# Performance work log

Hardware: AMD Instinct MI355X
Metric: run time of the kernel (lower is better)

Reference implementation:

```python
import jax, jax.numpy as jnp
import numpy as np

N = 50000        # nodes
E = 800000       # edges (avg degree 16)
IN = 128         # in_feats
HF = 128         # h_feats
HID = (IN + HF) // 2  # 128, per math.floor((h_feats+in_feats)/2)


def setup_inputs() -> dict:
    key = jax.random.key(0)
    ks = jax.random.split(key, 13)

    def glorot(k, fan_in, fan_out):
        s = (2.0 / (fan_in + fan_out)) ** 0.5
        return jax.random.normal(k, (fan_in, fan_out), jnp.float32) * s

    dims = [(IN, HID), (HID, HID), (HID, HID), (HID, HID), (HID, HF)]
    inp = {
        "in_feat": jax.random.normal(ks[0], (N, IN), jnp.float32),
        "src": jax.random.randint(ks[1], (E,), 0, N),
        "dst": jax.random.randint(ks[2], (E,), 0, N),
    }
    for i, (a, b) in enumerate(dims):
        inp[f"W{i+1}"] = glorot(ks[3 + i], a, b)
        inp[f"b{i+1}"] = jnp.zeros((b,), jnp.float32)
    return inp


def reference(in_feat, src, dst, W1, W2, W3, W4, W5, b1, b2, b3, b4, b5):
    # DGL GraphConv, norm='both': y = D_in^{-1/2} * A^T * (D_out^{-1/2} * x) @ W + b
    ones = jnp.ones((src.shape[0],), in_feat.dtype)
    deg_out = jnp.clip(jax.ops.segment_sum(ones, src, num_segments=N), 1.0)
    deg_in = jnp.clip(jax.ops.segment_sum(ones, dst, num_segments=N), 1.0)
    ns = (deg_out ** -0.5)[:, None]  # source-side norm [N,1]
    nd = (deg_in ** -0.5)[:, None]   # dest-side norm   [N,1]

    def conv(x, W, b):
        m = jax.ops.segment_sum((x * ns)[src], dst, num_segments=N)  # [N,D]
        return (m * nd) @ W + b

    h = in_feat
    for W, b in ((W1, b1), (W2, b2), (W3, b3), (W4, b4), (W5, b5)):
        h = jax.nn.relu(conv(h, W, b))

    # vectorized version of the per-element Python double loop threshold
    h_clone = jnp.where(h >= 0.5, jnp.float32(1.0), jnp.float32(0.0))
    return h, h_clone
```

## Files before the change

kernel.cpp:

```cpp
#include <hip/hip_runtime.h>

#define FEAT 128
#define RANGE 12800
#define NSLICE 64

typedef _Float16 half8 __attribute__((ext_vector_type(8)));
typedef _Float16 half4v __attribute__((ext_vector_type(4)));
typedef float f32x4 __attribute__((ext_vector_type(4)));

__global__ __launch_bounds__(1024) void hist_kernel(const int* __restrict__ src,
                                                    const int* __restrict__ dst,
                                                    unsigned* __restrict__ partialD,
                                                    unsigned* __restrict__ partialS,
                                                    int E, int NP) {
    __shared__ unsigned hpk[RANGE / 2];
    int per = (NP / RANGE) * NSLICE;
    int b = blockIdx.x;
    int halfsel = b / per;
    int q = b % per;
    int r = q / NSLICE;
    int s = q % NSLICE;
    const int* arr = halfsel ? src : dst;
    unsigned* out = halfsel ? partialS : partialD;
    int v0 = r * RANGE;
    int tid = threadIdx.x;
    for (int i = tid; i < RANGE / 2; i += 1024) hpk[i] = 0;
    __syncthreads();
    int e0 = (int)((long long)E * s / NSLICE);
    int e1 = (int)((long long)E * (s + 1) / NSLICE);
    for (int e = e0 + tid; e < e1; e += 1024) {
        unsigned d = (unsigned)(arr[e] - v0);
        if (d < RANGE) atomicAdd(&hpk[d >> 1], (d & 1) ? 65536u : 1u);
    }
    __syncthreads();
    size_t wbase = ((size_t)s * NP + v0) >> 1;
    for (int i = tid; i < RANGE / 2; i += 1024) out[wbase + i] = hpk[i];
}

__global__ __launch_bounds__(256) void scanp1_kernel(const unsigned short* __restrict__ pD,
                                                     const unsigned short* __restrict__ pS,
                                                     int* __restrict__ blockSums,
                                                     float* __restrict__ ns,
                                                     float* __restrict__ nd,
                                                     int NP, int n) {
    __shared__ int buf[256];
    int tid = threadIdx.x;
    int v = blockIdx.x * 256 + tid;
    int ssum = 0, osum = 0;
    #pragma unroll
    for (int s = 0; s < NSLICE; ++s) {
        ssum += pD[(size_t)s * NP + v];
        osum += pS[(size_t)s * NP + v];
    }
    if (v < n) {
        ns[v] = 1.0f / sqrtf((float)(osum < 1 ? 1 : osum));
        nd[v] = 1.0f / sqrtf((float)(ssum < 1 ? 1 : ssum));
    }
    buf[tid] = ssum;
    __syncthreads();
    #pragma unroll
    for (int off = 1; off < 256; off <<= 1) {
        int t = (tid >= off) ? buf[tid - off] : 0;
        __syncthreads();
        buf[tid] += t;
        __syncthreads();
    }
    if (tid == 255) blockSums[blockIdx.x] = buf[255];
}

__global__ __launch_bounds__(256) void scanp2_kernel(const int* __restrict__ blockSums,
                                                     int* __restrict__ blockOffs, int nb) {
    __shared__ int buf[256];
    int tid = threadIdx.x;
    int v = (tid < nb) ? blockSums[tid] : 0;
    buf[tid] = v;
    __syncthreads();
    #pragma unroll
    for (int off = 1; off < 256; off <<= 1) {
        int t = (tid >= off) ? buf[tid - off] : 0;
        __syncthreads();
        buf[tid] += t;
        __syncthreads();
    }
    if (tid < nb) blockOffs[tid] = buf[tid] - v;
}

__global__ __launch_bounds__(256) void scanp3_kernel(const unsigned short* __restrict__ pD,
                                                     const int* __restrict__ blockOffs,
                                                     int* __restrict__ cursorV,
                                                     int* __restrict__ offsc,
                                                     int NP, int n) {
    __shared__ int buf[256];
    int tid = threadIdx.x;
    int v = blockIdx.x * 256 + tid;
    int ssum = 0;
    #pragma unroll
    for (int s = 0; s < NSLICE; ++s) ssum += pD[(size_t)s * NP + v];
    buf[tid] = ssum;
    __syncthreads();
    #pragma unroll
    for (int off = 1; off < 256; off <<= 1) {
        int t = (tid >= off) ? buf[tid - off] : 0;
        __syncthreads();
        buf[tid] += t;
        __syncthreads();
    }
    int o = blockOffs[blockIdx.x] + buf[tid] - ssum;
    if (v <= n) offsc[v] = o;
    int* cv = cursorV + (size_t)v * NSLICE;
    #pragma unroll
    for (int s = 0; s < NSLICE; ++s) {
        int val = pD[(size_t)s * NP + v];
        cv[s] = o;
        o += val;
    }
}

__global__ __launch_bounds__(1024) void fill_kernel(const int* __restrict__ src,
                                                    const int* __restrict__ dst,
                                                    const int* __restrict__ cursorV,
                                                    int* __restrict__ esrc, int E, int NP) {
    __shared__ int cur[RANGE];
    int b = blockIdx.x;
    int r = b / NSLICE;
    int inner = b % NSLICE;
    int s = ((inner & 7) << 3) | (inner >> 3);
    int v0 = r * RANGE;
    int tid = threadIdx.x;
    for (int i = tid; i < RANGE; i += 1024)
        cur[i] = cursorV[(size_t)(v0 + i) * NSLICE + s];
    __syncthreads();
    int e0 = (int)((long long)E * s / NSLICE);
    int e1 = (int)((long long)E * (s + 1) / NSLICE);
    for (int e = e0 + tid; e < e1; e += 1024) {
        unsigned dd = (unsigned)(dst[e] - v0);
        if (dd < RANGE) {
            int p = atomicAdd(&cur[dd], 1);
            esrc[p] = src[e];
        }
    }
}

__global__ void prescale_kernel(const float* __restrict__ x, const float* __restrict__ ns,
                                _Float16* __restrict__ xh, int n) {
    int i = blockIdx.x * blockDim.x + threadIdx.x;
    if (i >= n * (FEAT / 8)) return;
    int v = i >> 4;
    float w = ns[v];
    float4 t0 = ((const float4*)x)[i * 2];
    float4 t1 = ((const float4*)x)[i * 2 + 1];
    half8 h;
    h[0] = (_Float16)(t0.x * w); h[1] = (_Float16)(t0.y * w);
    h[2] = (_Float16)(t0.z * w); h[3] = (_Float16)(t0.w * w);
    h[4] = (_Float16)(t1.x * w); h[5] = (_Float16)(t1.y * w);
    h[6] = (_Float16)(t1.z * w); h[7] = (_Float16)(t1.w * w);
    ((float4*)xh)[i] = __builtin_bit_cast(float4, h);
}

__global__ __launch_bounds__(256) void wprep_kernel(const float* __restrict__ Wa,
                                                    const float* __restrict__ Wb,
                                                    const float* __restrict__ Wc,
                                                    const float* __restrict__ Wd,
                                                    const float* __restrict__ We,
                                                    _Float16* __restrict__ w16t,
                                                    _Float16* __restrict__ wrt) {
    int gid = blockIdx.x * 256 + threadIdx.x;
    int l = gid >> 14;
    int idx = gid & 16383;
    int col = idx >> 7;
    int k = idx & 127;
    const float* Wp = (l == 0) ? Wa : (l == 1) ? Wb : (l == 2) ? Wc : (l == 3) ? Wd : We;
    float w = Wp[k * FEAT + col];
    _Float16 h = (_Float16)w;
    _Float16 r = (_Float16)(w - (float)h);
    w16t[gid] = h;
    wrt[gid] = r;
}

__global__ __launch_bounds__(256) void agg_kernel(const _Float16* __restrict__ x,
                                                  const int* __restrict__ offs,
                                                  const int* __restrict__ esrc,
                                                  const float* __restrict__ nd,
                                                  float* __restrict__ m, int n) {
    int gid = blockIdx.x * blockDim.x + threadIdx.x;
    int v = gid >> 6;
    if (v >= n) return;
    int lane = threadIdx.x & 63;
    int q = lane >> 4;
    int c = lane & 15;
    int s0 = offs[v], s1 = offs[v + 1];
    float a0[8] = {0,0,0,0,0,0,0,0};
    float a1[8] = {0,0,0,0,0,0,0,0};
    float a2[8] = {0,0,0,0,0,0,0,0};
    float a3[8] = {0,0,0,0,0,0,0,0};
    int j = s0 + q;
    for (; j + 12 < s1; j += 16) {
        int e0 = esrc[j], e1 = esrc[j + 4], e2 = esrc[j + 8], e3 = esrc[j + 12];
        float4 r0 = ((const float4*)(x + (size_t)e0 * FEAT))[c];
        float4 r1 = ((const float4*)(x + (size_t)e1 * FEAT))[c];
        float4 r2 = ((const float4*)(x + (size_t)e2 * FEAT))[c];
        float4 r3 = ((const float4*)(x + (size_t)e3 * FEAT))[c];
        half8 h0 = __builtin_bit_cast(half8, r0);
        half8 h1 = __builtin_bit_cast(half8, r1);
        half8 h2 = __builtin_bit_cast(half8, r2);
        half8 h3 = __builtin_bit_cast(half8, r3);
        #pragma unroll
        for (int k = 0; k < 8; ++k) {
            a0[k] += (float)h0[k];
            a1[k] += (float)h1[k];
            a2[k] += (float)h2[k];
            a3[k] += (float)h3[k];
        }
    }
    for (; j < s1; j += 4) {
        int e0 = esrc[j];
        float4 r0 = ((const float4*)(x + (size_t)e0 * FEAT))[c];
        half8 h0 = __builtin_bit_cast(half8, r0);
        #pragma unroll
        for (int k = 0; k < 8; ++k) a0[k] += (float)h0[k];
    }
    float r[8];
    #pragma unroll
    for (int k = 0; k < 8; ++k) r[k] = (a0[k] + a1[k]) + (a2[k] + a3[k]);
    #pragma unroll
    for (int k = 0; k < 8; ++k) {
        r[k] += __shfl_xor(r[k], 16);
        r[k] += __shfl_xor(r[k], 32);
    }
    if (lane < 16) {
        float sc = nd[v];
        float4 o0, o1;
        o0.x = r[0] * sc; o0.y = r[1] * sc; o0.z = r[2] * sc; o0.w = r[3] * sc;
        o1.x = r[4] * sc; o1.y = r[5] * sc; o1.z = r[6] * sc; o1.w = r[7] * sc;
        ((float4*)(m + (size_t)v * FEAT))[c * 2] = o0;
        ((float4*)(m + (size_t)v * FEAT))[c * 2 + 1] = o1;
    }
}

template<int MODE>
__global__ __launch_bounds__(256) void gemm_kernel(const float* __restrict__ M,
                                                   const _Float16* __restrict__ w16t,
                                                   const _Float16* __restrict__ wrt,
                                                   const float* __restrict__ bias,
                                                   const float* __restrict__ nsv,
                                                   _Float16* __restrict__ outh,
                                                   float* __restrict__ outf,
                                                   float* __restrict__ out2, int n) {
    __shared__ _Float16 A16s[32 * 128];
    __shared__ _Float16 Ars[32 * 128];
    __shared__ _Float16 W16s[128 * 128];
    __shared__ _Float16 Wrs[128 * 128];
    int tid = threadIdx.x;
    int r0 = blockIdx.x * 32;

    #pragma unroll
    for (int j = 0; j < 8; ++j) {
        int i = tid + j * 256;
        int col = i >> 4, ch = i & 15;
        int d = col * 16 + (ch ^ (col & 7));
        ((float4*)W16s)[d] = ((const float4*)w16t)[i];
        ((float4*)Wrs)[d]  = ((const float4*)wrt)[i];
    }
    #pragma unroll
    for (int j = 0; j < 4; ++j) {
        int i = tid + j * 256;
        int row = i >> 5, c4 = i & 31;
        int gr = r0 + row;
        float4 v = make_float4(0.f, 0.f, 0.f, 0.f);
        if (gr < n) v = ((const float4*)(M + (size_t)gr * FEAT))[c4];
        half4v h, rr;
        h[0] = (_Float16)v.x; h[1] = (_Float16)v.y; h[2] = (_Float16)v.z; h[3] = (_Float16)v.w;
        rr[0] = (_Float16)(v.x - (float)h[0]); rr[1] = (_Float16)(v.y - (float)h[1]);
        rr[2] = (_Float16)(v.z - (float)h[2]); rr[3] = (_Float16)(v.w - (float)h[3]);
        int d = row * 128 + (((c4 >> 1) ^ (row & 7)) << 3) + ((c4 & 1) << 2);
        *(half4v*)(A16s + d) = h;
        *(half4v*)(Ars + d) = rr;
    }
    __syncthreads();

    int lane = tid & 63;
    int w = tid >> 6;
    int l15 = lane & 15;
    int q = lane >> 4;
    int rbase = (w & 1) * 16 + l15;
    int cbase = (w >> 1) * 64;

    f32x4 acc[4] = {{0.f,0.f,0.f,0.f},{0.f,0.f,0.f,0.f},{0.f,0.f,0.f,0.f},{0.f,0.f,0.f,0.f}};
    #pragma unroll
    for (int ks = 0; ks < 4; ++ks) {
        int chunk = ks * 4 + q;
        int aoff = rbase * 128 + ((chunk ^ (rbase & 7)) << 3);
        half8 a16 = *(const half8*)(A16s + aoff);
        half8 ar  = *(const half8*)(Ars + aoff);
        #pragma unroll
        for (int ct = 0; ct < 4; ++ct) {
            int col = cbase + ct * 16 + l15;
            int boff = col * 128 + ((chunk ^ (col & 7)) << 3);
            half8 b16 = *(const half8*)(W16s + boff);
            half8 br  = *(const half8*)(Wrs + boff);
            acc[ct] = __builtin_amdgcn_mfma_f32_16x16x32_f16(a16, b16, acc[ct], 0, 0, 0);
            acc[ct] = __builtin_amdgcn_mfma_f32_16x16x32_f16(a16, br,  acc[ct], 0, 0, 0);
            acc[ct] = __builtin_amdgcn_mfma_f32_16x16x32_f16(ar,  b16, acc[ct], 0, 0, 0);
        }
    }

    int rloc = (w & 1) * 16 + q * 4;
    float scv[4];
    #pragma unroll
    for (int reg = 0; reg < 4; ++reg) {
        int row = r0 + rloc + reg;
        scv[reg] = (MODE == 0 && row < n) ? nsv[row] : 1.0f;
    }
    #pragma unroll
    for (int ct = 0; ct < 4; ++ct) {
        int col = cbase + ct * 16 + l15;
        float b = bias[col];
        #pragma unroll
        for (int reg = 0; reg < 4; ++reg) {
            int row = r0 + rloc + reg;
            if (row < n) {
                float h = acc[ct][reg] + b;
                h = h > 0.f ? h : 0.f;
                if (MODE == 0) {
                    outh[(size_t)row * FEAT + col] = (_Float16)(h * scv[reg]);
                } else {
                    outf[(size_t)row * FEAT + col] = h;
                    out2[(size_t)row * FEAT + col] = h >= 0.5f ? 1.f : 0.f;
                }
            }
        }
    }
}

extern "C" void kernel_launch(void* const* d_in, const int* in_sizes, int n_in,
                              void* d_out, int out_size, void* d_ws, size_t ws_size,
                              hipStream_t stream) {
    const float* in_feat = (const float*)d_in[0];
    const int*   src     = (const int*)d_in[1];
    const int*   dst     = (const int*)d_in[2];
    const float* W[5] = {(const float*)d_in[3], (const float*)d_in[5], (const float*)d_in[7],
                         (const float*)d_in[9], (const float*)d_in[11]};
    const float* B[5] = {(const float*)d_in[4], (const float*)d_in[6], (const float*)d_in[8],
                         (const float*)d_in[10], (const float*)d_in[12]};
    const int E = in_sizes[1];
    const int N = in_sizes[0] / FEAT;
    const int NRANGE = (N + RANGE - 1) / RANGE;
    const int NP = NRANGE * RANGE;
    const size_t MTOT = (size_t)NP * NSLICE;

    char* ws = (char*)d_ws;
    size_t off = 0;
    auto alloc = [&](size_t bytes) { size_t o = off; off += (bytes + 255) & ~size_t(255); return o; };
    unsigned* partialD = (unsigned*)(ws + alloc(MTOT * 2));
    size_t    pS_off   = alloc(MTOT * 2);
    unsigned* partialS = (unsigned*)(ws + pS_off);
    int*      esrc     = (int*)(ws + pS_off);
    size_t    cV_off   = alloc(MTOT * 4);
    int*      cursorV  = (int*)(ws + cV_off);
    _Float16* xh       = (_Float16*)(ws + cV_off);
    float*    ns       = (float*)(ws + alloc((size_t)N * 4));
    float*    nd       = (float*)(ws + alloc((size_t)N * 4));
    int*      offsc    = (int*)(ws + alloc((size_t)(N + 1) * 4));
    int*      blockSums = (int*)(ws + alloc(1024));
    int*      blockOffs = (int*)(ws + alloc(1024));
    _Float16* w16t     = (_Float16*)(ws + alloc(5 * 16384 * 2));
    _Float16* wrt      = (_Float16*)(ws + alloc(5 * 16384 * 2));

    float* out_h = (float*)d_out;
    float* out_c = out_h + (size_t)N * FEAT;

    const int histBlocks = 2 * NRANGE * NSLICE;
    const int scanBlocks = NP / 256;
    hist_kernel<<<histBlocks, 1024, 0, stream>>>(src, dst, partialD, partialS, E, NP);
    scanp1_kernel<<<scanBlocks, 256, 0, stream>>>((const unsigned short*)partialD,
                                                  (const unsigned short*)partialS,
                                                  blockSums, ns, nd, NP, N);
    scanp2_kernel<<<1, 256, 0, stream>>>(blockSums, blockOffs, scanBlocks);
    scanp3_kernel<<<scanBlocks, 256, 0, stream>>>((const unsigned short*)partialD,
                                                  blockOffs, cursorV, offsc, NP, N);
    fill_kernel<<<NRANGE * NSLICE, 1024, 0, stream>>>(src, dst, cursorV, esrc, E, NP);
    wprep_kernel<<<320, 256, 0, stream>>>(W[0], W[1], W[2], W[3], W[4], w16t, wrt);
    prescale_kernel<<<(N * (FEAT / 8) + 255) / 256, 256, 0, stream>>>(in_feat, ns, xh, N);

    const int agg_blocks = (int)(((size_t)N * 64 + 255) / 256);
    const int gemm_blocks = (N + 31) / 32;

    for (int l = 0; l < 5; ++l) {
        agg_kernel<<<agg_blocks, 256, 0, stream>>>(xh, offsc, esrc, nd, out_h, N);
        if (l < 4)
            gemm_kernel<0><<<gemm_blocks, 256, 0, stream>>>(out_h, w16t + (size_t)l * 16384,
                                                            wrt + (size_t)l * 16384, B[l], ns,
                                                            xh, nullptr, nullptr, N);
        else
            gemm_kernel<1><<<gemm_blocks, 256, 0, stream>>>(out_h, w16t + (size_t)l * 16384,
                                                            wrt + (size_t)l * 16384, B[l], nullptr,
                                                            nullptr, out_h, out_c, N);
    }
}
```

Measured before the change: 465.5 us.

## Fuse neighbor aggregation and dense GEMM into one per-layer kernel

Merges the aggregation kernel and the MFMA GEMM kernel into a single kernel per layer. Aggregated rows for a 64-node tile are kept in shared memory as fp32, then split into fp16 hi/lo and fed to the MFMAs, which removes the fp32 round trip of the aggregate through global memory and one launch per layer. Weights are now read straight from global memory instead of being staged in LDS. Ping-pong fp16 feature buffers are added because the layer now reads and writes features in the same kernel, at the cost of an extra N×128 workspace buffer.

```diff
diff --git a/kernel.cpp b/kernel.cpp
--- a/kernel.cpp
+++ b/kernel.cpp
@@ -5,7 +5,6 @@
 #define NSLICE 64
 
 typedef _Float16 half8 __attribute__((ext_vector_type(8)));
-typedef _Float16 half4v __attribute__((ext_vector_type(4)));
 typedef float f32x4 __attribute__((ext_vector_type(4)));
 
 __global__ __launch_bounds__(1024) void hist_kernel(const int* __restrict__ src,
@@ -177,134 +176,118 @@
     wrt[gid] = r;
 }
 
-__global__ __launch_bounds__(256) void agg_kernel(const _Float16* __restrict__ x,
-                                                  const int* __restrict__ offs,
-                                                  const int* __restrict__ esrc,
-                                                  const float* __restrict__ nd,
-                                                  float* __restrict__ m, int n) {
-    int gid = blockIdx.x * blockDim.x + threadIdx.x;
-    int v = gid >> 6;
-    if (v >= n) return;
-    int lane = threadIdx.x & 63;
+template<int MODE>
+__global__ __launch_bounds__(512, 4) void fused_kernel(const _Float16* __restrict__ x,
+                                                       const int* __restrict__ offs,
+                                                       const int* __restrict__ esrc,
+                                                       const float* __restrict__ nd,
+                                                       const float* __restrict__ nsv,
+                                                       const _Float16* __restrict__ w16t,
+                                                       const _Float16* __restrict__ wrt,
+                                                       const float* __restrict__ bias,
+                                                       _Float16* __restrict__ outh,
+                                                       float* __restrict__ outf,
+                                                       float* __restrict__ out2, int n) {
+    __shared__ float ms[64][132];
+    int tid = threadIdx.x;
+    int r0 = blockIdx.x * 64;
+
+    int hw = tid >> 5;
+    int lane = tid & 31;
     int q = lane >> 4;
     int c = lane & 15;
-    int s0 = offs[v], s1 = offs[v + 1];
-    float a0[8] = {0,0,0,0,0,0,0,0};
-    float a1[8] = {0,0,0,0,0,0,0,0};
-    float a2[8] = {0,0,0,0,0,0,0,0};
-    float a3[8] = {0,0,0,0,0,0,0,0};
-    int j = s0 + q;
-    for (; j + 12 < s1; j += 16) {
-        int e0 = esrc[j], e1 = esrc[j + 4], e2 = esrc[j + 8], e3 = esrc[j + 12];
-        float4 r0 = ((const float4*)(x + (size_t)e0 * FEAT))[c];
-        float4 r1 = ((const float4*)(x + (size_t)e1 * FEAT))[c];
-        float4 r2 = ((const float4*)(x + (size_t)e2 * FEAT))[c];
-        float4 r3 = ((const float4*)(x + (size_t)e3 * FEAT))[c];
-        half8 h0 = __builtin_bit_cast(half8, r0);
-        half8 h1 = __builtin_bit_cast(half8, r1);
-        half8 h2 = __builtin_bit_cast(half8, r2);
-        half8 h3 = __builtin_bit_cast(half8, r3);
-        #pragma unroll
-        for (int k = 0; k < 8; ++k) {
-            a0[k] += (float)h0[k];
-            a1[k] += (float)h1[k];
-            a2[k] += (float)h2[k];
-            a3[k] += (float)h3[k];
+    #pragma unroll
+    for (int t = 0; t < 4; ++t) {
+        int row = hw * 4 + t;
+        int v = r0 + row;
+        if (v < n) {
+            int s0 = offs[v], s1 = offs[v + 1];
+            float a0[8] = {0,0,0,0,0,0,0,0};
+            float a1[8] = {0,0,0,0,0,0,0,0};
+            float a2[8] = {0,0,0,0,0,0,0,0};
+            float a3[8] = {0,0,0,0,0,0,0,0};
+            int j = s0 + q;
+            for (; j + 6 < s1; j += 8) {
+                int e0 = esrc[j], e1 = esrc[j + 2], e2 = esrc[j + 4], e3 = esrc[j + 6];
+                float4 r0v = ((const float4*)(x + (size_t)e0 * FEAT))[c];
+                float4 r1v = ((const float4*)(x + (size_t)e1 * FEAT))[c];
+                float4 r2v = ((const float4*)(x + (size_t)e2 * FEAT))[c];
+                float4 r3v = ((const float4*)(x + (size_t)e3 * FEAT))[c];
+                half8 h0 = __builtin_bit_cast(half8, r0v);
+                half8 h1 = __builtin_bit_cast(half8, r1v);
+                half8 h2 = __builtin_bit_cast(half8, r2v);
+                half8 h3 = __builtin_bit_cast(half8, r3v);
+                #pragma unroll
+                for (int k = 0; k < 8; ++k) {
+                    a0[k] += (float)h0[k];
+                    a1[k] += (float)h1[k];
+                    a2[k] += (float)h2[k];
+                    a3[k] += (float)h3[k];
+                }
+            }
+            for (; j < s1; j += 2) {
+                int e0 = esrc[j];
+                float4 r0v = ((const float4*)(x + (size_t)e0 * FEAT))[c];
+                half8 h0 = __builtin_bit_cast(half8, r0v);
+                #pragma unroll
+                for (int k = 0; k < 8; ++k) a0[k] += (float)h0[k];
+            }
+            float r[8];
+            #pragma unroll
+            for (int k = 0; k < 8; ++k) r[k] = (a0[k] + a1[k]) + (a2[k] + a3[k]);
+            #pragma unroll
+            for (int k = 0; k < 8; ++k) r[k] += __shfl_xor(r[k], 16);
+            if (q == 0) {
+                float sc = nd[v];
+                float4 o0, o1;
+                o0.x = r[0] * sc; o0.y = r[1] * sc; o0.z = r[2] * sc; o0.w = r[3] * sc;
+                o1.x = r[4] * sc; o1.y = r[5] * sc; o1.z = r[6] * sc; o1.w = r[7] * sc;
+                *(float4*)&ms[row][c * 8] = o0;
+                *(float4*)&ms[row][c * 8 + 4] = o1;
+            }
+        } else if (q == 0) {
+            float4 z = make_float4(0.f, 0.f, 0.f, 0.f);
+            *(float4*)&ms[row][c * 8] = z;
+            *(float4*)&ms[row][c * 8 + 4] = z;
         }
     }
-    for (; j < s1; j += 4) {
-        int e0 = esrc[j];
-        float4 r0 = ((const float4*)(x + (size_t)e0 * FEAT))[c];
-        half8 h0 = __builtin_bit_cast(half8, r0);
-        #pragma unroll
-        for (int k = 0; k < 8; ++k) a0[k] += (float)h0[k];
-    }
-    float r[8];
-    #pragma unroll
-    for (int k = 0; k < 8; ++k) r[k] = (a0[k] + a1[k]) + (a2[k] + a3[k]);
-    #pragma unroll
-    for (int k = 0; k < 8; ++k) {
-        r[k] += __shfl_xor(r[k], 16);
-        r[k] += __shfl_xor(r[k], 32);
-    }
-    if (lane < 16) {
-        float sc = nd[v];
-        float4 o0, o1;
-        o0.x = r[0] * sc; o0.y = r[1] * sc; o0.z = r[2] * sc; o0.w = r[3] * sc;
-        o1.x = r[4] * sc; o1.y = r[5] * sc; o1.z = r[6] * sc; o1.w = r[7] * sc;
-        ((float4*)(m + (size_t)v * FEAT))[c * 2] = o0;
-        ((float4*)(m + (size_t)v * FEAT))[c * 2 + 1] = o1;
-    }
-}
-
-template<int MODE>
-__global__ __launch_bounds__(256) void gemm_kernel(const float* __restrict__ M,
-                                                   const _Float16* __restrict__ w16t,
-                                                   const _Float16* __restrict__ wrt,
-                                                   const float* __restrict__ bias,
-                                                   const float* __restrict__ nsv,
-                                                   _Float16* __restrict__ outh,
-                                                   float* __restrict__ outf,
-                                                   float* __restrict__ out2, int n) {
-    __shared__ _Float16 A16s[32 * 128];
-    __shared__ _Float16 Ars[32 * 128];
-    __shared__ _Float16 W16s[128 * 128];
-    __shared__ _Float16 Wrs[128 * 128];
-    int tid = threadIdx.x;
-    int r0 = blockIdx.x * 32;
-
-    #pragma unroll
-    for (int j = 0; j < 8; ++j) {
-        int i = tid + j * 256;
-        int col = i >> 4, ch = i & 15;
-        int d = col * 16 + (ch ^ (col & 7));
-        ((float4*)W16s)[d] = ((const float4*)w16t)[i];
-        ((float4*)Wrs)[d]  = ((const float4*)wrt)[i];
-    }
-    #pragma unroll
-    for (int j = 0; j < 4; ++j) {
-        int i = tid + j * 256;
-        int row = i >> 5, c4 = i & 31;
-        int gr = r0 + row;
-        float4 v = make_float4(0.f, 0.f, 0.f, 0.f);
-        if (gr < n) v = ((const float4*)(M + (size_t)gr * FEAT))[c4];
-        half4v h, rr;
-        h[0] = (_Float16)v.x; h[1] = (_Float16)v.y; h[2] = (_Float16)v.z; h[3] = (_Float16)v.w;
-        rr[0] = (_Float16)(v.x - (float)h[0]); rr[1] = (_Float16)(v.y - (float)h[1]);
-        rr[2] = (_Float16)(v.z - (float)h[2]); rr[3] = (_Float16)(v.w - (float)h[3]);
-        int d = row * 128 + (((c4 >> 1) ^ (row & 7)) << 3) + ((c4 & 1) << 2);
-        *(half4v*)(A16s + d) = h;
-        *(half4v*)(Ars + d) = rr;
-    }
-    __syncthreads();
-
-    int lane = tid & 63;
+    __syncthreads();
+
+    int lane64 = tid & 63;
     int w = tid >> 6;
-    int l15 = lane & 15;
-    int q = lane >> 4;
-    int rbase = (w & 1) * 16 + l15;
-    int cbase = (w >> 1) * 64;
+    int l15 = lane64 & 15;
+    int qq = lane64 >> 4;
+    int rw = w & 3, cw = w >> 2;
+    int rbase = rw * 16 + l15;
+    int cbase = cw * 64;
 
     f32x4 acc[4] = {{0.f,0.f,0.f,0.f},{0.f,0.f,0.f,0.f},{0.f,0.f,0.f,0.f},{0.f,0.f,0.f,0.f}};
     #pragma unroll
     for (int ks = 0; ks < 4; ++ks) {
-        int chunk = ks * 4 + q;
-        int aoff = rbase * 128 + ((chunk ^ (rbase & 7)) << 3);
-        half8 a16 = *(const half8*)(A16s + aoff);
-        half8 ar  = *(const half8*)(Ars + aoff);
+        int chunk = ks * 4 + qq;
+        float4 f0 = *(const float4*)&ms[rbase][chunk * 8];
+        float4 f1 = *(const float4*)&ms[rbase][chunk * 8 + 4];
+        half8 a16, ar;
+        a16[0] = (_Float16)f0.x; a16[1] = (_Float16)f0.y;
+        a16[2] = (_Float16)f0.z; a16[3] = (_Float16)f0.w;
+        a16[4] = (_Float16)f1.x; a16[5] = (_Float16)f1.y;
+        a16[6] = (_Float16)f1.z; a16[7] = (_Float16)f1.w;
+        ar[0] = (_Float16)(f0.x - (float)a16[0]); ar[1] = (_Float16)(f0.y - (float)a16[1]);
+        ar[2] = (_Float16)(f0.z - (float)a16[2]); ar[3] = (_Float16)(f0.w - (float)a16[3]);
+        ar[4] = (_Float16)(f1.x - (float)a16[4]); ar[5] = (_Float16)(f1.y - (float)a16[5]);
+        ar[6] = (_Float16)(f1.z - (float)a16[6]); ar[7] = (_Float16)(f1.w - (float)a16[7]);
         #pragma unroll
         for (int ct = 0; ct < 4; ++ct) {
             int col = cbase + ct * 16 + l15;
-            int boff = col * 128 + ((chunk ^ (col & 7)) << 3);
-            half8 b16 = *(const half8*)(W16s + boff);
-            half8 br  = *(const half8*)(Wrs + boff);
+            half8 b16 = *(const half8*)(w16t + (size_t)col * FEAT + chunk * 8);
+            half8 br  = *(const half8*)(wrt  + (size_t)col * FEAT + chunk * 8);
             acc[ct] = __builtin_amdgcn_mfma_f32_16x16x32_f16(a16, b16, acc[ct], 0, 0, 0);
             acc[ct] = __builtin_amdgcn_mfma_f32_16x16x32_f16(a16, br,  acc[ct], 0, 0, 0);
             acc[ct] = __builtin_amdgcn_mfma_f32_16x16x32_f16(ar,  b16, acc[ct], 0, 0, 0);
         }
     }
 
-    int rloc = (w & 1) * 16 + q * 4;
+    int rloc = rw * 16 + qq * 4;
     float scv[4];
     #pragma unroll
     for (int reg = 0; reg < 4; ++reg) {
@@ -357,7 +340,7 @@
     int*      esrc     = (int*)(ws + pS_off);
     size_t    cV_off   = alloc(MTOT * 4);
     int*      cursorV  = (int*)(ws + cV_off);
-    _Float16* xh       = (_Float16*)(ws + cV_off);
+    _Float16* xhA      = (_Float16*)(ws + cV_off);
     float*    ns       = (float*)(ws + alloc((size_t)N * 4));
     float*    nd       = (float*)(ws + alloc((size_t)N * 4));
     int*      offsc    = (int*)(ws + alloc((size_t)(N + 1) * 4));
@@ -365,6 +348,7 @@
     int*      blockOffs = (int*)(ws + alloc(1024));
     _Float16* w16t     = (_Float16*)(ws + alloc(5 * 16384 * 2));
     _Float16* wrt      = (_Float16*)(ws + alloc(5 * 16384 * 2));
+    _Float16* xhB      = (_Float16*)(ws + alloc((size_t)N * FEAT * 2));
 
     float* out_h = (float*)d_out;
     float* out_c = out_h + (size_t)N * FEAT;
@@ -380,20 +364,22 @@
                                                   blockOffs, cursorV, offsc, NP, N);
     fill_kernel<<<NRANGE * NSLICE, 1024, 0, stream>>>(src, dst, cursorV, esrc, E, NP);
     wprep_kernel<<<320, 256, 0, stream>>>(W[0], W[1], W[2], W[3], W[4], w16t, wrt);
-    prescale_kernel<<<(N * (FEAT / 8) + 255) / 256, 256, 0, stream>>>(in_feat, ns, xh, N);
-
-    const int agg_blocks = (int)(((size_t)N * 64 + 255) / 256);
-    const int gemm_blocks = (N + 31) / 32;
+    prescale_kernel<<<(N * (FEAT / 8) + 255) / 256, 256, 0, stream>>>(in_feat, ns, xhA, N);
+
+    const int fusedBlocks = (N + 63) / 64;
 
     for (int l = 0; l < 5; ++l) {
-        agg_kernel<<<agg_blocks, 256, 0, stream>>>(xh, offsc, esrc, nd, out_h, N);
+        const _Float16* xin = (l & 1) ? xhB : xhA;
+        _Float16*       xout = (l & 1) ? xhA : xhB;
         if (l < 4)
-            gemm_kernel<0><<<gemm_blocks, 256, 0, stream>>>(out_h, w16t + (size_t)l * 16384,
-                                                            wrt + (size_t)l * 16384, B[l], ns,
-                                                            xh, nullptr, nullptr, N);
+            fused_kernel<0><<<fusedBlocks, 512, 0, stream>>>(xin, offsc, esrc, nd, ns,
+                                                             w16t + (size_t)l * 16384,
+                                                             wrt + (size_t)l * 16384, B[l],
+                                                             xout, nullptr, nullptr, N);
         else
-            gemm_kernel<1><<<gemm_blocks, 256, 0, stream>>>(out_h, w16t + (size_t)l * 16384,
-                                                            wrt + (size_t)l * 16384, B[l], nullptr,
-                                                            nullptr, out_h, out_c, N);
-    }
-}
+            fused_kernel<1><<<fusedBlocks, 512, 0, stream>>>(xin, offsc, esrc, nd, nullptr,
+                                                             w16t + (size_t)l * 16384,
+                                                             wrt + (size_t)l * 16384, B[l],
+                                                             nullptr, out_h, out_c, N);
+    }
+}
```

New measurement: 514.0 us. +10.4%, slower.

## Merge prep kernels and read GEMM weights from global instead of LDS

Applied to the files above, without the earlier changes.

Folds the weight-prep work into the first scan kernel and merges the block-sum scan into the third scan kernel, so the preprocessing chain issues two fewer launches. The GEMM kernel now uses 512 threads on 64-row tiles and stops staging the two 128x128 fp16 weight tiles in shared memory. B fragments are loaded straight from global/L2 instead, which cuts LDS use from about 80KB to 32KB per block and allows more resident blocks. The trade-off is more scattered global loads of the weight matrices inside the MFMA loop, and every prep2 block redundantly rescans the block sums.

```diff
diff --git a/kernel.cpp b/kernel.cpp
--- a/kernel.cpp
+++ b/kernel.cpp
@@ -37,26 +37,69 @@
     for (int i = tid; i < RANGE / 2; i += 1024) out[wbase + i] = hpk[i];
 }
 
-__global__ __launch_bounds__(256) void scanp1_kernel(const unsigned short* __restrict__ pD,
-                                                     const unsigned short* __restrict__ pS,
-                                                     int* __restrict__ blockSums,
-                                                     float* __restrict__ ns,
-                                                     float* __restrict__ nd,
-                                                     int NP, int n) {
+__global__ __launch_bounds__(256) void prep1_kernel(const unsigned short* __restrict__ pD,
+                                                    const unsigned short* __restrict__ pS,
+                                                    int* __restrict__ blockSums,
+                                                    float* __restrict__ ns,
+                                                    float* __restrict__ nd,
+                                                    const float* __restrict__ Wa,
+                                                    const float* __restrict__ Wb,
+                                                    const float* __restrict__ Wc,
+                                                    const float* __restrict__ Wd,
+                                                    const float* __restrict__ We,
+                                                    _Float16* __restrict__ w16t,
+                                                    _Float16* __restrict__ wrt,
+                                                    int NP, int n, int sb) {
+    int tid = threadIdx.x;
+    int b = blockIdx.x;
+    if (b < sb) {
+        __shared__ int buf[256];
+        int v = b * 256 + tid;
+        int ssum = 0, osum = 0;
+        #pragma unroll
+        for (int s = 0; s < NSLICE; ++s) {
+            ssum += pD[(size_t)s * NP + v];
+            osum += pS[(size_t)s * NP + v];
+        }
+        if (v < n) {
+            ns[v] = 1.0f / sqrtf((float)(osum < 1 ? 1 : osum));
+            nd[v] = 1.0f / sqrtf((float)(ssum < 1 ? 1 : ssum));
+        }
+        buf[tid] = ssum;
+        __syncthreads();
+        #pragma unroll
+        for (int off = 1; off < 256; off <<= 1) {
+            int t = (tid >= off) ? buf[tid - off] : 0;
+            __syncthreads();
+            buf[tid] += t;
+            __syncthreads();
+        }
+        if (tid == 255) blockSums[b] = buf[255];
+    } else {
+        int gid = (b - sb) * 256 + tid;
+        int l = gid >> 14;
+        int idx = gid & 16383;
+        int col = idx >> 7;
+        int k = idx & 127;
+        const float* Wp = (l == 0) ? Wa : (l == 1) ? Wb : (l == 2) ? Wc : (l == 3) ? Wd : We;
+        float w = Wp[k * FEAT + col];
+        _Float16 h = (_Float16)w;
+        _Float16 r = (_Float16)(w - (float)h);
+        w16t[gid] = h;
+        wrt[gid] = r;
+    }
+}
+
+__global__ __launch_bounds__(256) void prep2_kernel(const unsigned short* __restrict__ pD,
+                                                    const int* __restrict__ blockSums,
+                                                    int* __restrict__ cursorV,
+                                                    int* __restrict__ offsc,
+                                                    int NP, int n, int nb) {
     __shared__ int buf[256];
     int tid = threadIdx.x;
-    int v = blockIdx.x * 256 + tid;
-    int ssum = 0, osum = 0;
-    #pragma unroll
-    for (int s = 0; s < NSLICE; ++s) {
-        ssum += pD[(size_t)s * NP + v];
-        osum += pS[(size_t)s * NP + v];
-    }
-    if (v < n) {
-        ns[v] = 1.0f / sqrtf((float)(osum < 1 ? 1 : osum));
-        nd[v] = 1.0f / sqrtf((float)(ssum < 1 ? 1 : ssum));
-    }
-    buf[tid] = ssum;
+    int b = blockIdx.x;
+    int bsv = (tid < nb) ? blockSums[tid] : 0;
+    buf[tid] = bsv;
     __syncthreads();
     #pragma unroll
     for (int off = 1; off < 256; off <<= 1) {
@@ -65,15 +108,13 @@
         buf[tid] += t;
         __syncthreads();
     }
-    if (tid == 255) blockSums[blockIdx.x] = buf[255];
-}
-
-__global__ __launch_bounds__(256) void scanp2_kernel(const int* __restrict__ blockSums,
-                                                     int* __restrict__ blockOffs, int nb) {
-    __shared__ int buf[256];
-    int tid = threadIdx.x;
-    int v = (tid < nb) ? blockSums[tid] : 0;
-    buf[tid] = v;
+    int myoff = (b > 0) ? buf[b - 1] : 0;
+    __syncthreads();
+    int v = b * 256 + tid;
+    int ssum = 0;
+    #pragma unroll
+    for (int s = 0; s < NSLICE; ++s) ssum += pD[(size_t)s * NP + v];
+    buf[tid] = ssum;
     __syncthreads();
     #pragma unroll
     for (int off = 1; off < 256; off <<= 1) {
@@ -82,30 +123,7 @@
         buf[tid] += t;
         __syncthreads();
     }
-    if (tid < nb) blockOffs[tid] = buf[tid] - v;
-}
-
-__global__ __launch_bounds__(256) void scanp3_kernel(const unsigned short* __restrict__ pD,
-                                                     const int* __restrict__ blockOffs,
-                                                     int* __restrict__ cursorV,
-                                                     int* __restrict__ offsc,
-                                                     int NP, int n) {
-    __shared__ int buf[256];
-    int tid = threadIdx.x;
-    int v = blockIdx.x * 256 + tid;
-    int ssum = 0;
-    #pragma unroll
-    for (int s = 0; s < NSLICE; ++s) ssum += pD[(size_t)s * NP + v];
-    buf[tid] = ssum;
-    __syncthreads();
-    #pragma unroll
-    for (int off = 1; off < 256; off <<= 1) {
-        int t = (tid >= off) ? buf[tid - off] : 0;
-        __syncthreads();
-        buf[tid] += t;
-        __syncthreads();
-    }
-    int o = blockOffs[blockIdx.x] + buf[tid] - ssum;
+    int o = myoff + buf[tid] - ssum;
     if (v <= n) offsc[v] = o;
     int* cv = cursorV + (size_t)v * NSLICE;
     #pragma unroll
@@ -155,26 +173,6 @@
     h[4] = (_Float16)(t1.x * w); h[5] = (_Float16)(t1.y * w);
     h[6] = (_Float16)(t1.z * w); h[7] = (_Float16)(t1.w * w);
     ((float4*)xh)[i] = __builtin_bit_cast(float4, h);
-}
-
-__global__ __launch_bounds__(256) void wprep_kernel(const float* __restrict__ Wa,
-                                                    const float* __restrict__ Wb,
-                                                    const float* __restrict__ Wc,
-                                                    const float* __restrict__ Wd,
-                                                    const float* __restrict__ We,
-                                                    _Float16* __restrict__ w16t,
-                                                    _Float16* __restrict__ wrt) {
-    int gid = blockIdx.x * 256 + threadIdx.x;
-    int l = gid >> 14;
-    int idx = gid & 16383;
-    int col = idx >> 7;
-    int k = idx & 127;
-    const float* Wp = (l == 0) ? Wa : (l == 1) ? Wb : (l == 2) ? Wc : (l == 3) ? Wd : We;
-    float w = Wp[k * FEAT + col];
-    _Float16 h = (_Float16)w;
-    _Float16 r = (_Float16)(w - (float)h);
-    w16t[gid] = h;
-    wrt[gid] = r;
 }
 
 __global__ __launch_bounds__(256) void agg_kernel(const _Float16* __restrict__ x,
@@ -238,32 +236,22 @@
 }
 
 template<int MODE>
-__global__ __launch_bounds__(256) void gemm_kernel(const float* __restrict__ M,
-                                                   const _Float16* __restrict__ w16t,
-                                                   const _Float16* __restrict__ wrt,
-                                                   const float* __restrict__ bias,
-                                                   const float* __restrict__ nsv,
-                                                   _Float16* __restrict__ outh,
-                                                   float* __restrict__ outf,
-                                                   float* __restrict__ out2, int n) {
-    __shared__ _Float16 A16s[32 * 128];
-    __shared__ _Float16 Ars[32 * 128];
-    __shared__ _Float16 W16s[128 * 128];
-    __shared__ _Float16 Wrs[128 * 128];
-    int tid = threadIdx.x;
-    int r0 = blockIdx.x * 32;
-
-    #pragma unroll
-    for (int j = 0; j < 8; ++j) {
-        int i = tid + j * 256;
-        int col = i >> 4, ch = i & 15;
-        int d = col * 16 + (ch ^ (col & 7));
-        ((float4*)W16s)[d] = ((const float4*)w16t)[i];
-        ((float4*)Wrs)[d]  = ((const float4*)wrt)[i];
-    }
-    #pragma unroll
-    for (int j = 0; j < 4; ++j) {
-        int i = tid + j * 256;
+__global__ __launch_bounds__(512, 4) void gemm_kernel(const float* __restrict__ M,
+                                                      const _Float16* __restrict__ w16t,
+                                                      const _Float16* __restrict__ wrt,
+                                                      const float* __restrict__ bias,
+                                                      const float* __restrict__ nsv,
+                                                      _Float16* __restrict__ outh,
+                                                      float* __restrict__ outf,
+                                                      float* __restrict__ out2, int n) {
+    __shared__ _Float16 A16s[64 * 128];
+    __shared__ _Float16 Ars[64 * 128];
+    int tid = threadIdx.x;
+    int r0 = blockIdx.x * 64;
+
+    #pragma unroll
+    for (int jj = 0; jj < 4; ++jj) {
+        int i = tid + jj * 512;
         int row = i >> 5, c4 = i & 31;
         int gr = r0 + row;
         float4 v = make_float4(0.f, 0.f, 0.f, 0.f);
@@ -278,33 +266,33 @@
     }
     __syncthreads();
 
-    int lane = tid & 63;
+    int lane64 = tid & 63;
     int w = tid >> 6;
-    int l15 = lane & 15;
-    int q = lane >> 4;
-    int rbase = (w & 1) * 16 + l15;
-    int cbase = (w >> 1) * 64;
+    int l15 = lane64 & 15;
+    int qq = lane64 >> 4;
+    int rw = w & 3, cw = w >> 2;
+    int rbase = rw * 16 + l15;
+    int cbase = cw * 64;
 
     f32x4 acc[4] = {{0.f,0.f,0.f,0.f},{0.f,0.f,0.f,0.f},{0.f,0.f,0.f,0.f},{0.f,0.f,0.f,0.f}};
     #pragma unroll
     for (int ks = 0; ks < 4; ++ks) {
-        int chunk = ks * 4 + q;
+        int chunk = ks * 4 + qq;
         int aoff = rbase * 128 + ((chunk ^ (rbase & 7)) << 3);
         half8 a16 = *(const half8*)(A16s + aoff);
         half8 ar  = *(const half8*)(Ars + aoff);
         #pragma unroll
         for (int ct = 0; ct < 4; ++ct) {
             int col = cbase + ct * 16 + l15;
-            int boff = col * 128 + ((chunk ^ (col & 7)) << 3);
-            half8 b16 = *(const half8*)(W16s + boff);
-            half8 br  = *(const half8*)(Wrs + boff);
+            half8 b16 = *(const half8*)(w16t + (size_t)col * FEAT + chunk * 8);
+            half8 br  = *(const half8*)(wrt  + (size_t)col * FEAT + chunk * 8);
             acc[ct] = __builtin_amdgcn_mfma_f32_16x16x32_f16(a16, b16, acc[ct], 0, 0, 0);
             acc[ct] = __builtin_amdgcn_mfma_f32_16x16x32_f16(a16, br,  acc[ct], 0, 0, 0);
             acc[ct] = __builtin_amdgcn_mfma_f32_16x16x32_f16(ar,  b16, acc[ct], 0, 0, 0);
         }
     }
 
-    int rloc = (w & 1) * 16 + q * 4;
+    int rloc = rw * 16 + qq * 4;
     float scv[4];
     #pragma unroll
     for (int reg = 0; reg < 4; ++reg) {
@@ -362,7 +350,6 @@
     float*    nd       = (float*)(ws + alloc((size_t)N * 4));
     int*      offsc    = (int*)(ws + alloc((size_t)(N + 1) * 4));
     int*      blockSums = (int*)(ws + alloc(1024));
-    int*      blockOffs = (int*)(ws + alloc(1024));
     _Float16* w16t     = (_Float16*)(ws + alloc(5 * 16384 * 2));
     _Float16* wrt      = (_Float16*)(ws + alloc(5 * 16384 * 2));
 
@@ -371,28 +358,29 @@
 
     const int histBlocks = 2 * NRANGE * NSLICE;
     const int scanBlocks = NP / 256;
+
     hist_kernel<<<histBlocks, 1024, 0, stream>>>(src, dst, partialD, partialS, E, NP);
-    scanp1_kernel<<<scanBlocks, 256, 0, stream>>>((const unsigned short*)partialD,
-                                                  (const unsigned short*)partialS,
-                                                  blockSums, ns, nd, NP, N);
-    scanp2_kernel<<<1, 256, 0, stream>>>(blockSums, blockOffs, scanBlocks);
-    scanp3_kernel<<<scanBlocks, 256, 0, stream>>>((const unsigned short*)partialD,
-                                                  blockOffs, cursorV, offsc, NP, N);
+    prep1_kernel<<<scanBlocks + 320, 256, 0, stream>>>((const unsigned short*)partialD,
+                                                       (const unsigned short*)partialS,
+                                                       blockSums, ns, nd,
+                                                       W[0], W[1], W[2], W[3], W[4],
+                                                       w16t, wrt, NP, N, scanBlocks);
+    prep2_kernel<<<scanBlocks, 256, 0, stream>>>((const unsigned short*)partialD, blockSums,
+                                                 cursorV, offsc, NP, N, scanBlocks);
     fill_kernel<<<NRANGE * NSLICE, 1024, 0, stream>>>(src, dst, cursorV, esrc, E, NP);
-    wprep_kernel<<<320, 256, 0, stream>>>(W[0], W[1], W[2], W[3], W[4], w16t, wrt);
     prescale_kernel<<<(N * (FEAT / 8) + 255) / 256, 256, 0, stream>>>(in_feat, ns, xh, N);
 
     const int agg_blocks = (int)(((size_t)N * 64 + 255) / 256);
-    const int gemm_blocks = (N + 31) / 32;
+    const int gemm_blocks = (N + 63) / 64;
 
     for (int l = 0; l < 5; ++l) {
         agg_kernel<<<agg_blocks, 256, 0, stream>>>(xh, offsc, esrc, nd, out_h, N);
         if (l < 4)
-            gemm_kernel<0><<<gemm_blocks, 256, 0, stream>>>(out_h, w16t + (size_t)l * 16384,
+            gemm_kernel<0><<<gemm_blocks, 512, 0, stream>>>(out_h, w16t + (size_t)l * 16384,
                                                             wrt + (size_t)l * 16384, B[l], ns,
                                                             xh, nullptr, nullptr, N);
         else
-            gemm_kernel<1><<<gemm_blocks, 256, 0, stream>>>(out_h, w16t + (size_t)l * 16384,
+            gemm_kernel<1><<<gemm_blocks, 512, 0, stream>>>(out_h, w16t + (size_t)l * 16384,
                                                             wrt + (size_t)l * 16384, B[l], nullptr,
                                                             nullptr, out_h, out_c, N);
     }
```

After: 530.2 us. 1.14x slower.
